# Optimization experiments

Hardware: AMD Instinct MI355X
Metric: run time of the kernel (lower is better)

The kernel has to match this reference:

```python
import jax, jax.numpy as jnp
import numpy as np

N_GROUPS = 32
EPS = 1e-5
N_HEADS = 4
D_K = 64


def group_norm(x, gamma, beta):
    # x: [B, C, H, W]; normalize over (channels within group, spatial)
    B, C, H, W = x.shape
    xg = x.reshape(B, N_GROUPS, C // N_GROUPS, H, W)
    mean = jnp.mean(xg, axis=(2, 3, 4), keepdims=True)
    var = jnp.var(xg, axis=(2, 3, 4), keepdims=True)
    xn = ((xg - mean) * jax.lax.rsqrt(var + EPS)).reshape(B, C, H, W)
    return xn * gamma[None, :, None, None] + beta[None, :, None, None]


def setup_inputs() -> dict:
    key = jax.random.key(0)
    ks = jax.random.split(key, 4)
    B, C, H, W = 4, 256, 64, 64
    x = jax.random.normal(ks[0], (B, C, H, W), dtype=jnp.float32)
    gamma = jnp.ones((C,), dtype=jnp.float32)
    beta = jnp.zeros((C,), dtype=jnp.float32)
    w_qkv = jax.random.normal(ks[1], (C, N_HEADS * D_K * 3), dtype=jnp.float32) * (C ** -0.5)
    b_qkv = jnp.zeros((N_HEADS * D_K * 3,), dtype=jnp.float32)
    w_out = jax.random.normal(ks[2], (N_HEADS * D_K, C), dtype=jnp.float32) * ((N_HEADS * D_K) ** -0.5)
    b_out = jnp.zeros((C,), dtype=jnp.float32)
    return {"x": x, "gamma": gamma, "beta": beta, "w_qkv": w_qkv,
            "b_qkv": b_qkv, "w_out": w_out, "b_out": b_out}


def reference(x, gamma, beta, w_qkv, b_qkv, w_out, b_out):
    B, C, H, W = x.shape
    S = H * W
    scale = D_K ** -0.5
    # GroupNorm -> [B, S, C]
    h = group_norm(x, gamma, beta).reshape(B, C, S).transpose(0, 2, 1)
    qkv = (h @ w_qkv + b_qkv).reshape(B, S, N_HEADS, 3 * D_K)
    q, k, v = jnp.split(qkv, 3, axis=-1)          # each [B, S, H, D]
    attn = jnp.einsum('bihd,bjhd->bijh', q, k) * scale
    attn = jax.nn.softmax(attn, axis=2)           # softmax over j (keys)
    res = jnp.einsum('bijh,bjhd->bihd', attn, v)  # [B, S, H, D]
    res = res.reshape(B, S, N_HEADS * D_K)
    res = res @ w_out + b_out                     # [B, S, C]
    res = res.transpose(0, 2, 1).reshape(B, C, H, W)
    return res + x
```

## Files before the change

### kernel.cpp

```cpp
#include <hip/hip_runtime.h>
#include <hip/hip_bf16.h>


typedef __attribute__((ext_vector_type(8))) short short8;
typedef __attribute__((ext_vector_type(4))) float f32x4;
typedef __attribute__((ext_vector_type(16))) float f32x16;

__device__ __forceinline__ unsigned short f2bf(float f) {
    union { float f; unsigned u; } v; v.f = f;
    unsigned r = v.u + 0x7FFF + ((v.u >> 16) & 1);
    return (unsigned short)(r >> 16);
}

__device__ __forceinline__ unsigned cvt_pk_bf16(float lo, float hi) {
    unsigned r;
    asm("v_cvt_pk_bf16_f32 %0, %1, %2" : "=v"(r) : "v"(lo), "v"(hi));
    return r;
}

__device__ __forceinline__ void permswap(unsigned &x, unsigned &y) {
    asm("v_permlane32_swap_b32 %0, %1" : "+v"(x), "+v"(y));
}

__device__ __forceinline__ float fexp2(float x) {
    float r;
    asm("v_exp_f32 %0, %1" : "=v"(r) : "v"(x));
    return r;
}

__device__ __forceinline__ void gl_lds16(const void* g, void* l) {
    __builtin_amdgcn_global_load_lds(
        (const __attribute__((address_space(1))) void*)(g),
        (__attribute__((address_space(3))) void*)(l), 16, 0, 0);
}

__device__ __forceinline__ f32x16 fzero16() {
    f32x16 z;
    #pragma unroll
    for (int i = 0; i < 16; ++i) z[i] = 0.f;
    return z;
}

__global__ __launch_bounds__(1024) void k_gn_stats(const float* __restrict__ x,
                                                   float* __restrict__ stats) {
    int bg = blockIdx.x;
    const float4* xp = (const float4*)(x + bg * 32768);
    float s1 = 0.f, s2 = 0.f;
    for (int i = threadIdx.x; i < 8192; i += 1024) {
        float4 v = xp[i];
        s1 += v.x + v.y + v.z + v.w;
        s2 += v.x*v.x + v.y*v.y + v.z*v.z + v.w*v.w;
    }
    #pragma unroll
    for (int off = 32; off; off >>= 1) {
        s1 += __shfl_down(s1, off);
        s2 += __shfl_down(s2, off);
    }
    __shared__ float r1[16], r2[16];
    int wid = threadIdx.x >> 6;
    if ((threadIdx.x & 63) == 0) { r1[wid] = s1; r2[wid] = s2; }
    __syncthreads();
    if (threadIdx.x == 0) {
        float a = 0.f, b = 0.f;
        #pragma unroll
        for (int i = 0; i < 16; ++i) { a += r1[i]; b += r2[i]; }
        float mean = a * (1.f/32768.f);
        float var  = b * (1.f/32768.f) - mean*mean;
        stats[bg*2]   = mean;
        stats[bg*2+1] = rsqrtf(var + 1e-5f);
    }
}

__global__ void k_cvt_w(const float* __restrict__ wqkv, const float* __restrict__ wout,
                        unsigned short* __restrict__ wqkvT, unsigned short* __restrict__ woutT) {
    int i = blockIdx.x * 256 + threadIdx.x;
    if (i < 196608) {
        int k = i / 768, n = i - k * 768;
        wqkvT[n*256 + k] = f2bf(wqkv[i]);
    }
    if (i < 65536) {
        int k = i >> 8, n = i & 255;
        woutT[n*256 + k] = f2bf(wout[i]);
    }
}

__global__ __launch_bounds__(256) void k_gn_norm(
    const float* __restrict__ x, const float* __restrict__ gamma,
    const float* __restrict__ beta, const float* __restrict__ stats,
    unsigned short* __restrict__ h) {
    __shared__ unsigned short t[64][72];
    int s0 = blockIdx.x * 64, c0 = blockIdx.y * 64, b = blockIdx.z;
    int tid = threadIdx.x;
    int sl = (tid & 15) * 4;
    int cr = tid >> 4;
    #pragma unroll
    for (int p = 0; p < 4; ++p) {
        int c = c0 + cr + p * 16;
        float4 v = *(const float4*)&x[(b*256 + c)*4096 + s0 + sl];
        int sg = (b*32 + (c >> 3)) * 2;
        float mean = stats[sg], rstd = stats[sg+1];
        float sa = rstd * gamma[c];
        float sb = beta[c] - mean * sa;
        ushort4 pk;
        pk.x = f2bf(v.x*sa + sb); pk.y = f2bf(v.y*sa + sb);
        pk.z = f2bf(v.z*sa + sb); pk.w = f2bf(v.w*sa + sb);
        *(ushort4*)&t[cr + p*16][sl] = pk;
    }
    __syncthreads();
    int sr = tid >> 2;
    int cc = (tid & 3) * 16;
    unsigned rr[8];
    #pragma unroll
    for (int j = 0; j < 8; ++j)
        rr[j] = (unsigned)t[cc + 2*j][sr] | ((unsigned)t[cc + 2*j + 1][sr] << 16);
    unsigned short* hp = &h[(b*4096 + s0 + sr)*256 + c0];
    *(uint4*)&hp[cc]     = make_uint4(rr[0], rr[1], rr[2], rr[3]);
    *(uint4*)&hp[cc + 8] = make_uint4(rr[4], rr[5], rr[6], rr[7]);
}

__global__ __launch_bounds__(256) void k_qkv(
    const unsigned short* __restrict__ h, const unsigned short* __restrict__ wT,
    const float* __restrict__ bqkv,
    unsigned short* __restrict__ q, unsigned short* __restrict__ kk,
    unsigned short* __restrict__ vT) {
    int mt = blockIdx.x, head = blockIdx.y;
    int tid = threadIdx.x;
    int wid = tid >> 6, lane = tid & 63;
    int g = lane >> 4, li = lane & 15;
    int m0 = mt * 64 + wid * 16;
    int row = m0 + li;
    f32x4 acc[12];
    #pragma unroll
    for (int nt = 0; nt < 12; ++nt) acc[nt] = (f32x4){0.f,0.f,0.f,0.f};
    #pragma unroll
    for (int kt = 0; kt < 8; ++kt) {
        short8 a = *(const short8*)&h[row*256 + kt*32 + g*8];
        #pragma unroll
        for (int nt = 0; nt < 12; ++nt) {
            int n = head*192 + nt*16 + li;
            short8 b = *(const short8*)&wT[n*256 + kt*32 + g*8];
            acc[nt] = __builtin_amdgcn_mfma_f32_16x16x32_bf16(a, b, acc[nt], 0, 0, 0);
        }
    }
    int b = m0 >> 12;
    int s0 = m0 & 4095;
    int bh = b*4 + head;
    #pragma unroll
    for (int nt = 0; nt < 12; ++nt) {
        int ng = head*192 + nt*16 + li;
        float bias = bqkv[ng];
        int d = (nt & 3)*16 + li;
        if ((nt >> 2) == 2) {
            ushort4 pk;
            pk.x = f2bf(acc[nt][0] + bias); pk.y = f2bf(acc[nt][1] + bias);
            pk.z = f2bf(acc[nt][2] + bias); pk.w = f2bf(acc[nt][3] + bias);
            *(ushort4*)&vT[(bh*64 + d)*4096 + s0 + g*4] = pk;
        } else if ((nt >> 2) == 0) {
            #pragma unroll
            for (int r = 0; r < 4; ++r)
                q[(bh*4096 + s0 + g*4 + r)*64 + d] = f2bf((acc[nt][r] + bias) * 0.1803368801f);
        } else {
            #pragma unroll
            for (int r = 0; r < 4; ++r)
                kk[(bh*4096 + s0 + g*4 + r)*64 + d] = f2bf(acc[nt][r] + bias);
        }
    }
}

__global__ __launch_bounds__(512, 4) void k_attn(
    const unsigned short* __restrict__ q, const unsigned short* __restrict__ kk,
    const unsigned short* __restrict__ vT, unsigned short* __restrict__ ao) {
    __shared__ __align__(16) char smem[65536];

    int n = blockIdx.x;
    int qt = n >> 4;
    int bh = ((n & 7) << 1) | ((n >> 3) & 1);
    int tid = threadIdx.x;
    int wid = tid >> 6, lane = tid & 63;
    int qw = wid & 3, st = wid >> 2;
    int hi = lane >> 5, il = lane & 31;
    int swl = (il & 7) << 4;

    int qbase = qt * 128 + qw * 32;
    int qrow = bh * 4096 + qbase + il;
    short8 bq[4];
    #pragma unroll
    for (int kc = 0; kc < 4; ++kc)
        bq[kc] = *(const short8*)&q[qrow*64 + kc*16 + hi*8];

    short8 ones;
    #pragma unroll
    for (int i = 0; i < 8; ++i) ones[i] = (short)0x3F80;

    unsigned p16  = tid * 16;
    unsigned row0 = p16 >> 7;
    unsigned sw   = (row0 & 7) << 4;
    unsigned ks0  = p16 ^ sw;
    unsigned vc0  = (p16 & 127u) ^ sw;
    const char* kbase = (const char*)kk + (size_t)bh * 524288;
    const char* vbase = (const char*)vT + (size_t)(bh*64 + row0) * 8192;
    unsigned woff = wid * 1024;

#define STAGE_PAIR(d, pair) do {                                             \
    const char* _k0 = kbase + (size_t)(2*(pair)) * 8192;                     \
    size_t _vo = (size_t)(2*(pair)) * 128;                                   \
    gl_lds16(_k0 + ks0,              smem + ((d)*2+0)*8192 + woff);          \
    gl_lds16(_k0 + 8192 + ks0,       smem + ((d)*2+1)*8192 + woff);          \
    gl_lds16(vbase + _vo + vc0,       smem + 32768 + ((d)*2+0)*8192 + woff); \
    gl_lds16(vbase + _vo + 128 + vc0, smem + 32768 + ((d)*2+1)*8192 + woff); \
} while (0)

    f32x16 o0 = fzero16(), o1 = fzero16(), accl = fzero16();
    float m_run = 0.f;

    STAGE_PAIR(0, 0);
    asm volatile("s_waitcnt vmcnt(0)" ::: "memory");
    __builtin_amdgcn_s_barrier();
    asm volatile("" ::: "memory");

    int cur = 0;
    for (int tp = 0; tp < 32; ++tp) {
        if (tp < 31) STAGE_PAIR(cur ^ 1, tp + 1);

        const char* kb = smem + (cur*2 + st) * 8192;
        const char* vb = smem + 32768 + (cur*2 + st) * 8192;

        float nm = -m_run;
        f32x16 p0, p1;
        #pragma unroll
        for (int r = 0; r < 16; ++r) { p0[r] = nm; p1[r] = nm; }
        __builtin_amdgcn_s_setprio(1);
        #pragma unroll
        for (int kc = 0; kc < 4; ++kc) {
            int c = (kc*32 + hi*16) ^ swl;
            short8 ka0 = *(const short8*)(kb + il*128 + c);
            short8 ka1 = *(const short8*)(kb + 4096 + il*128 + c);
            p0 = __builtin_amdgcn_mfma_f32_32x32x16_bf16(ka0, bq[kc], p0, 0, 0, 0);
            p1 = __builtin_amdgcn_mfma_f32_32x32x16_bf16(ka1, bq[kc], p1, 0, 0, 0);
        }
        __builtin_amdgcn_s_setprio(0);

        #pragma unroll
        for (int r = 0; r < 16; ++r) {
            p0[r] = fexp2(p0[r]);
            p1[r] = fexp2(p1[r]);
        }
        float m8[8];
        #pragma unroll
        for (int r = 0; r < 8; ++r)
            m8[r] = fmaxf(fmaxf(p0[2*r], p0[2*r+1]), fmaxf(p1[2*r], p1[2*r+1]));
        float pm = fmaxf(fmaxf(fmaxf(m8[0], m8[1]), fmaxf(m8[2], m8[3])),
                         fmaxf(fmaxf(m8[4], m8[5]), fmaxf(m8[6], m8[7])));
        if (__any(pm > 16.f)) {
            pm = fmaxf(pm, __shfl_xor(pm, 32));
            float fac = 1.f / pm;
            m_run += log2f(pm);
            accl[0] *= fac;
            #pragma unroll
            for (int r = 0; r < 16; ++r) {
                o0[r] *= fac; o1[r] *= fac;
                p0[r] *= fac; p1[r] *= fac;
            }
        }

        __builtin_amdgcn_s_setprio(1);
        #pragma unroll
        for (int jc = 0; jc < 4; ++jc) {
            const int hh = jc & 1;
            float e0, e1, e2, e3, e4, e5, e6, e7;
            if (jc < 2) {
                e0 = p0[hh*8+0]; e1 = p0[hh*8+1]; e2 = p0[hh*8+2]; e3 = p0[hh*8+3];
                e4 = p0[hh*8+4]; e5 = p0[hh*8+5]; e6 = p0[hh*8+6]; e7 = p0[hh*8+7];
            } else {
                e0 = p1[hh*8+0]; e1 = p1[hh*8+1]; e2 = p1[hh*8+2]; e3 = p1[hh*8+3];
                e4 = p1[hh*8+4]; e5 = p1[hh*8+5]; e6 = p1[hh*8+6]; e7 = p1[hh*8+7];
            }
            unsigned a = cvt_pk_bf16(e0, e1);
            unsigned b = cvt_pk_bf16(e2, e3);
            unsigned c = cvt_pk_bf16(e4, e5);
            unsigned d = cvt_pk_bf16(e6, e7);
            permswap(a, c);
            permswap(b, d);
            union { unsigned u[4]; short8 s8; } pb;
            pb.u[0] = a; pb.u[1] = b; pb.u[2] = c; pb.u[3] = d;
            int co = (jc*32 + hi*16) ^ swl;
            short8 va0 = *(const short8*)(vb + il*128 + co);
            short8 va1 = *(const short8*)(vb + 4096 + il*128 + co);
            o0   = __builtin_amdgcn_mfma_f32_32x32x16_bf16(va0, pb.s8, o0, 0, 0, 0);
            o1   = __builtin_amdgcn_mfma_f32_32x32x16_bf16(va1, pb.s8, o1, 0, 0, 0);
            accl = __builtin_amdgcn_mfma_f32_32x32x16_bf16(ones, pb.s8, accl, 0, 0, 0);
        }
        __builtin_amdgcn_s_setprio(0);

        if (tp < 31) asm volatile("s_waitcnt vmcnt(0)" ::: "memory");
        asm volatile("" ::: "memory");
        __builtin_amdgcn_s_barrier();
        asm volatile("" ::: "memory");
        cur ^= 1;
    }
#undef STAGE_PAIR

    float l_loc = accl[0];

    float* red = (float*)smem;
    int slot = ((qw*64 + lane) * 34);
    if (st == 1) {
        #pragma unroll
        for (int r = 0; r < 16; ++r) { red[slot + r] = o0[r]; red[slot + 16 + r] = o1[r]; }
        red[slot + 32] = l_loc;
        red[slot + 33] = m_run;
    }
    __syncthreads();
    if (st == 0) {
        float m1 = red[slot + 33], l1 = red[slot + 32];
        float m = fmaxf(m_run, m1);
        float f0 = fexp2(m_run - m), f1 = fexp2(m1 - m);
        float inv = 1.f / (l_loc * f0 + l1 * f1);
        float a0 = f0 * inv, a1 = f1 * inv;
        int b = bh >> 2, hh = bh & 3;
        int s = qbase + il;
        unsigned short* aop = &ao[((size_t)(b*4096 + s))*256 + hh*64];
        #pragma unroll
        for (int rr = 0; rr < 4; ++rr) {
            ushort4 pk0, pk1;
            pk0.x = f2bf(o0[rr*4+0]*a0 + red[slot + rr*4+0]*a1);
            pk0.y = f2bf(o0[rr*4+1]*a0 + red[slot + rr*4+1]*a1);
            pk0.z = f2bf(o0[rr*4+2]*a0 + red[slot + rr*4+2]*a1);
            pk0.w = f2bf(o0[rr*4+3]*a0 + red[slot + rr*4+3]*a1);
            *(ushort4*)&aop[rr*8 + hi*4] = pk0;
            pk1.x = f2bf(o1[rr*4+0]*a0 + red[slot + 16 + rr*4+0]*a1);
            pk1.y = f2bf(o1[rr*4+1]*a0 + red[slot + 16 + rr*4+1]*a1);
            pk1.z = f2bf(o1[rr*4+2]*a0 + red[slot + 16 + rr*4+2]*a1);
            pk1.w = f2bf(o1[rr*4+3]*a0 + red[slot + 16 + rr*4+3]*a1);
            *(ushort4*)&aop[32 + rr*8 + hi*4] = pk1;
        }
    }
}

__global__ __launch_bounds__(256) void k_out(
    const unsigned short* __restrict__ ao, const unsigned short* __restrict__ wT,
    const float* __restrict__ bout, const float* __restrict__ x,
    float* __restrict__ out) {
    int mt = blockIdx.x;
    int tid = threadIdx.x;
    int wid = tid >> 6, lane = tid & 63;
    int g = lane >> 4, li = lane & 15;
    int rg = wid & 1, ch = wid >> 1;
    int m0 = mt * 32 + rg * 16;
    int row = m0 + li;
    f32x4 acc[8];
    #pragma unroll
    for (int nt = 0; nt < 8; ++nt) acc[nt] = (f32x4){0.f,0.f,0.f,0.f};
    #pragma unroll
    for (int kt = 0; kt < 8; ++kt) {
        short8 a = *(const short8*)&ao[row*256 + kt*32 + g*8];
        #pragma unroll
        for (int nt = 0; nt < 8; ++nt) {
            int nn = ch*128 + nt*16 + li;
            short8 b = *(const short8*)&wT[nn*256 + kt*32 + g*8];
            acc[nt] = __builtin_amdgcn_mfma_f32_16x16x32_bf16(a, b, acc[nt], 0, 0, 0);
        }
    }
    int b = m0 >> 12;
    int s0 = (m0 & 4095) + g*4;
    #pragma unroll
    for (int nt = 0; nt < 8; ++nt) {
        int c = ch*128 + nt*16 + li;
        float bias = bout[c];
        int base = (b*256 + c)*4096 + s0;
        float4 xr = *(const float4*)&x[base];
        float4 ov;
        ov.x = acc[nt][0] + bias + xr.x;
        ov.y = acc[nt][1] + bias + xr.y;
        ov.z = acc[nt][2] + bias + xr.z;
        ov.w = acc[nt][3] + bias + xr.w;
        *(float4*)&out[base] = ov;
    }
}

extern "C" void kernel_launch(void* const* d_in, const int* in_sizes, int n_in,
                              void* d_out, int out_size, void* d_ws, size_t ws_size,
                              hipStream_t stream) {
    (void)in_sizes; (void)n_in; (void)out_size; (void)ws_size;
    const float* x     = (const float*)d_in[0];
    const float* gamma = (const float*)d_in[1];
    const float* beta  = (const float*)d_in[2];
    const float* wqkv  = (const float*)d_in[3];
    const float* bqkv  = (const float*)d_in[4];
    const float* wout  = (const float*)d_in[5];
    const float* bout  = (const float*)d_in[6];
    float* out = (float*)d_out;

    char* ws = (char*)d_ws;
    unsigned short* h     = (unsigned short*)(ws);
    unsigned short* q     = (unsigned short*)(ws + (8u<<20));
    unsigned short* kk    = (unsigned short*)(ws + (16u<<20));
    unsigned short* vT    = (unsigned short*)(ws + (24u<<20));
    unsigned short* ao    = (unsigned short*)(ws + (32u<<20));
    unsigned short* wqkvT = (unsigned short*)(ws + (40u<<20));
    unsigned short* woutT = (unsigned short*)(ws + (40u<<20) + 393216);
    float*          stats = (float*)(ws + (40u<<20) + 524288);

    k_gn_stats<<<128, 1024, 0, stream>>>(x, stats);
    k_cvt_w<<<768, 256, 0, stream>>>(wqkv, wout, wqkvT, woutT);
    k_gn_norm<<<dim3(64, 4, 4), 256, 0, stream>>>(x, gamma, beta, stats, h);
    k_qkv<<<dim3(256, 4), 256, 0, stream>>>(h, wqkvT, bqkv, q, kk, vT);
    k_attn<<<dim3(512), 512, 0, stream>>>(q, kk, vT, ao);
    k_out<<<dim3(512), 256, 0, stream>>>(ao, woutT, bout, x, out);
}
```

Before: 175.1 us.

## Fuse GroupNorm apply into QKV GEMM and merge stats with weight conversion

Merges the GroupNorm statistics and weight transpose/convert kernels into one launch split by block index. The normalize-and-transpose step now runs inside the QKV projection kernel, writing the normalized bf16 tile into LDS instead of a global h buffer. Each 512-thread block computes all 768 output columns for 64 rows, so x is read once per row tile. This cuts two launches and the h round trip through memory. In exchange there are fewer blocks (256), a heavier per-wave accumulator (24 tiles), and more LDS per block, which may lower occupancy.

```diff
diff --git a/kernel.cpp b/kernel.cpp
--- a/kernel.cpp
+++ b/kernel.cpp
@@ -41,128 +41,134 @@
     return z;
 }
 
-__global__ __launch_bounds__(1024) void k_gn_stats(const float* __restrict__ x,
-                                                   float* __restrict__ stats) {
-    int bg = blockIdx.x;
-    const float4* xp = (const float4*)(x + bg * 32768);
-    float s1 = 0.f, s2 = 0.f;
-    for (int i = threadIdx.x; i < 8192; i += 1024) {
-        float4 v = xp[i];
-        s1 += v.x + v.y + v.z + v.w;
-        s2 += v.x*v.x + v.y*v.y + v.z*v.z + v.w*v.w;
-    }
-    #pragma unroll
-    for (int off = 32; off; off >>= 1) {
-        s1 += __shfl_down(s1, off);
-        s2 += __shfl_down(s2, off);
-    }
-    __shared__ float r1[16], r2[16];
-    int wid = threadIdx.x >> 6;
-    if ((threadIdx.x & 63) == 0) { r1[wid] = s1; r2[wid] = s2; }
-    __syncthreads();
-    if (threadIdx.x == 0) {
-        float a = 0.f, b = 0.f;
-        #pragma unroll
-        for (int i = 0; i < 16; ++i) { a += r1[i]; b += r2[i]; }
-        float mean = a * (1.f/32768.f);
-        float var  = b * (1.f/32768.f) - mean*mean;
-        stats[bg*2]   = mean;
-        stats[bg*2+1] = rsqrtf(var + 1e-5f);
-    }
-}
-
-__global__ void k_cvt_w(const float* __restrict__ wqkv, const float* __restrict__ wout,
-                        unsigned short* __restrict__ wqkvT, unsigned short* __restrict__ woutT) {
-    int i = blockIdx.x * 256 + threadIdx.x;
-    if (i < 196608) {
-        int k = i / 768, n = i - k * 768;
-        wqkvT[n*256 + k] = f2bf(wqkv[i]);
-    }
-    if (i < 65536) {
-        int k = i >> 8, n = i & 255;
-        woutT[n*256 + k] = f2bf(wout[i]);
-    }
-}
-
-__global__ __launch_bounds__(256) void k_gn_norm(
+__global__ __launch_bounds__(1024) void k_pre(
+    const float* __restrict__ x, float* __restrict__ stats,
+    const float* __restrict__ wqkv, const float* __restrict__ wout,
+    unsigned short* __restrict__ wqkvT, unsigned short* __restrict__ woutT) {
+    if (blockIdx.x < 128) {
+        int bg = blockIdx.x;
+        const float4* xp = (const float4*)(x + bg * 32768);
+        float s1 = 0.f, s2 = 0.f;
+        for (int i = threadIdx.x; i < 8192; i += 1024) {
+            float4 v = xp[i];
+            s1 += v.x + v.y + v.z + v.w;
+            s2 += v.x*v.x + v.y*v.y + v.z*v.z + v.w*v.w;
+        }
+        #pragma unroll
+        for (int off = 32; off; off >>= 1) {
+            s1 += __shfl_down(s1, off);
+            s2 += __shfl_down(s2, off);
+        }
+        __shared__ float r1[16], r2[16];
+        int wid = threadIdx.x >> 6;
+        if ((threadIdx.x & 63) == 0) { r1[wid] = s1; r2[wid] = s2; }
+        __syncthreads();
+        if (threadIdx.x == 0) {
+            float a = 0.f, b = 0.f;
+            #pragma unroll
+            for (int i = 0; i < 16; ++i) { a += r1[i]; b += r2[i]; }
+            float mean = a * (1.f/32768.f);
+            float var  = b * (1.f/32768.f) - mean*mean;
+            stats[bg*2]   = mean;
+            stats[bg*2+1] = rsqrtf(var + 1e-5f);
+        }
+    } else {
+        int i = (blockIdx.x - 128) * 1024 + threadIdx.x;
+        if (i < 196608) {
+            int k = i / 768, n = i - k * 768;
+            wqkvT[n*256 + k] = f2bf(wqkv[i]);
+        }
+        if (i < 65536) {
+            int k = i >> 8, n = i & 255;
+            woutT[n*256 + k] = f2bf(wout[i]);
+        }
+    }
+}
+
+__global__ __launch_bounds__(512, 2) void k_qkvf(
     const float* __restrict__ x, const float* __restrict__ gamma,
     const float* __restrict__ beta, const float* __restrict__ stats,
-    unsigned short* __restrict__ h) {
-    __shared__ unsigned short t[64][72];
-    int s0 = blockIdx.x * 64, c0 = blockIdx.y * 64, b = blockIdx.z;
-    int tid = threadIdx.x;
-    int sl = (tid & 15) * 4;
-    int cr = tid >> 4;
-    #pragma unroll
-    for (int p = 0; p < 4; ++p) {
-        int c = c0 + cr + p * 16;
-        float4 v = *(const float4*)&x[(b*256 + c)*4096 + s0 + sl];
-        int sg = (b*32 + (c >> 3)) * 2;
-        float mean = stats[sg], rstd = stats[sg+1];
-        float sa = rstd * gamma[c];
-        float sb = beta[c] - mean * sa;
-        ushort4 pk;
-        pk.x = f2bf(v.x*sa + sb); pk.y = f2bf(v.y*sa + sb);
-        pk.z = f2bf(v.z*sa + sb); pk.w = f2bf(v.w*sa + sb);
-        *(ushort4*)&t[cr + p*16][sl] = pk;
-    }
-    __syncthreads();
-    int sr = tid >> 2;
-    int cc = (tid & 3) * 16;
-    unsigned rr[8];
-    #pragma unroll
-    for (int j = 0; j < 8; ++j)
-        rr[j] = (unsigned)t[cc + 2*j][sr] | ((unsigned)t[cc + 2*j + 1][sr] << 16);
-    unsigned short* hp = &h[(b*4096 + s0 + sr)*256 + c0];
-    *(uint4*)&hp[cc]     = make_uint4(rr[0], rr[1], rr[2], rr[3]);
-    *(uint4*)&hp[cc + 8] = make_uint4(rr[4], rr[5], rr[6], rr[7]);
-}
-
-__global__ __launch_bounds__(256) void k_qkv(
-    const unsigned short* __restrict__ h, const unsigned short* __restrict__ wT,
-    const float* __restrict__ bqkv,
+    const unsigned short* __restrict__ wT, const float* __restrict__ bqkv,
     unsigned short* __restrict__ q, unsigned short* __restrict__ kk,
     unsigned short* __restrict__ vT) {
-    int mt = blockIdx.x, head = blockIdx.y;
+    __shared__ unsigned short t[64][72];
+    __shared__ unsigned short lds_h[64][272];
+
+    int m0 = blockIdx.x * 64;
+    int b = m0 >> 12;
+    int s0 = m0 & 4095;
     int tid = threadIdx.x;
+
+    #pragma unroll
+    for (int cb = 0; cb < 4; ++cb) {
+        int c0 = cb * 64;
+        #pragma unroll
+        for (int k = 0; k < 2; ++k) {
+            int u = tid + k * 512;
+            int cr = u >> 4;
+            int sl = (u & 15) * 4;
+            int c = c0 + cr;
+            float4 v = *(const float4*)&x[(b*256 + c)*4096 + s0 + sl];
+            int sg = (b*32 + (c >> 3)) * 2;
+            float mean = stats[sg], rstd = stats[sg+1];
+            float sa = rstd * gamma[c];
+            float sb = beta[c] - mean * sa;
+            ushort4 pk;
+            pk.x = f2bf(v.x*sa + sb); pk.y = f2bf(v.y*sa + sb);
+            pk.z = f2bf(v.z*sa + sb); pk.w = f2bf(v.w*sa + sb);
+            *(ushort4*)&t[cr][sl] = pk;
+        }
+        __syncthreads();
+        int sr = tid >> 3;
+        int cc8 = (tid & 7) * 8;
+        unsigned rr[4];
+        #pragma unroll
+        for (int j = 0; j < 4; ++j)
+            rr[j] = (unsigned)t[cc8 + 2*j][sr] | ((unsigned)t[cc8 + 2*j + 1][sr] << 16);
+        *(uint4*)&lds_h[sr][c0 + cc8] = make_uint4(rr[0], rr[1], rr[2], rr[3]);
+        __syncthreads();
+    }
+
     int wid = tid >> 6, lane = tid & 63;
     int g = lane >> 4, li = lane & 15;
-    int m0 = mt * 64 + wid * 16;
-    int row = m0 + li;
-    f32x4 acc[12];
-    #pragma unroll
-    for (int nt = 0; nt < 12; ++nt) acc[nt] = (f32x4){0.f,0.f,0.f,0.f};
+    int rg = wid & 3, cg = wid >> 2;
+    int rowl = rg * 16 + li;
+    f32x4 acc[24];
+    #pragma unroll
+    for (int nt = 0; nt < 24; ++nt) acc[nt] = (f32x4){0.f,0.f,0.f,0.f};
     #pragma unroll
     for (int kt = 0; kt < 8; ++kt) {
-        short8 a = *(const short8*)&h[row*256 + kt*32 + g*8];
-        #pragma unroll
-        for (int nt = 0; nt < 12; ++nt) {
-            int n = head*192 + nt*16 + li;
-            short8 b = *(const short8*)&wT[n*256 + kt*32 + g*8];
-            acc[nt] = __builtin_amdgcn_mfma_f32_16x16x32_bf16(a, b, acc[nt], 0, 0, 0);
-        }
-    }
-    int b = m0 >> 12;
-    int s0 = m0 & 4095;
-    int bh = b*4 + head;
-    #pragma unroll
-    for (int nt = 0; nt < 12; ++nt) {
-        int ng = head*192 + nt*16 + li;
+        short8 a = *(const short8*)&lds_h[rowl][kt*32 + g*8];
+        #pragma unroll
+        for (int nt = 0; nt < 24; ++nt) {
+            int n = cg*384 + nt*16 + li;
+            short8 bb = *(const short8*)&wT[n*256 + kt*32 + g*8];
+            acc[nt] = __builtin_amdgcn_mfma_f32_16x16x32_bf16(a, bb, acc[nt], 0, 0, 0);
+        }
+    }
+    int m0w = m0 + rg * 16;
+    int s0w = m0w & 4095;
+    #pragma unroll
+    for (int nt = 0; nt < 24; ++nt) {
+        int ng = cg*384 + nt*16 + li;
+        int head = cg*2 + nt/12;
+        int ntl = nt % 12;
+        int bh = b*4 + head;
         float bias = bqkv[ng];
-        int d = (nt & 3)*16 + li;
-        if ((nt >> 2) == 2) {
+        int d = (ntl & 3)*16 + li;
+        if ((ntl >> 2) == 2) {
             ushort4 pk;
             pk.x = f2bf(acc[nt][0] + bias); pk.y = f2bf(acc[nt][1] + bias);
             pk.z = f2bf(acc[nt][2] + bias); pk.w = f2bf(acc[nt][3] + bias);
-            *(ushort4*)&vT[(bh*64 + d)*4096 + s0 + g*4] = pk;
-        } else if ((nt >> 2) == 0) {
+            *(ushort4*)&vT[(bh*64 + d)*4096 + s0w + g*4] = pk;
+        } else if ((ntl >> 2) == 0) {
             #pragma unroll
             for (int r = 0; r < 4; ++r)
-                q[(bh*4096 + s0 + g*4 + r)*64 + d] = f2bf((acc[nt][r] + bias) * 0.1803368801f);
+                q[(bh*4096 + s0w + g*4 + r)*64 + d] = f2bf((acc[nt][r] + bias) * 0.1803368801f);
         } else {
             #pragma unroll
             for (int r = 0; r < 4; ++r)
-                kk[(bh*4096 + s0 + g*4 + r)*64 + d] = f2bf(acc[nt][r] + bias);
+                kk[(bh*4096 + s0w + g*4 + r)*64 + d] = f2bf(acc[nt][r] + bias);
         }
     }
 }
@@ -392,7 +398,6 @@
     float* out = (float*)d_out;
 
     char* ws = (char*)d_ws;
-    unsigned short* h     = (unsigned short*)(ws);
     unsigned short* q     = (unsigned short*)(ws + (8u<<20));
     unsigned short* kk    = (unsigned short*)(ws + (16u<<20));
     unsigned short* vT    = (unsigned short*)(ws + (24u<<20));
@@ -401,10 +406,8 @@
     unsigned short* woutT = (unsigned short*)(ws + (40u<<20) + 393216);
     float*          stats = (float*)(ws + (40u<<20) + 524288);
 
-    k_gn_stats<<<128, 1024, 0, stream>>>(x, stats);
-    k_cvt_w<<<768, 256, 0, stream>>>(wqkv, wout, wqkvT, woutT);
-    k_gn_norm<<<dim3(64, 4, 4), 256, 0, stream>>>(x, gamma, beta, stats, h);
-    k_qkv<<<dim3(256, 4), 256, 0, stream>>>(h, wqkvT, bqkv, q, kk, vT);
+    k_pre<<<320, 1024, 0, stream>>>(x, stats, wqkv, wout, wqkvT, woutT);
+    k_qkvf<<<256, 512, 0, stream>>>(x, gamma, beta, stats, wqkvT, bqkv, q, kk, vT);
     k_attn<<<dim3(512), 512, 0, stream>>>(q, kk, vT, ao);
     k_out<<<dim3(512), 256, 0, stream>>>(ao, woutT, bout, x, out);
 }
```

Result: faster. 170.4 us (-2.7%).
